# Kernel tuning notes

Measured on AMD Instinct MI355X. Metric: run time of the kernel, lower is better.

## Reference

```python
import jax, jax.numpy as jnp
import numpy as np

N, D, K = 32768, 128, 16
EPS = 1e-8  # torch cosine_similarity eps


def setup_inputs() -> dict:
    key = jax.random.key(0)
    k1, k2, kW1, kW2, kV = jax.random.split(key, 5)
    # xavier_normal std for [K, fan_in, fan_out]-style tensors (torch treats dim0 as batch? no:
    # xavier_normal_ on a 3D tensor uses fan_in = D*1? torch computes fan from dims 1.. with receptive field.
    # fan_in = size(1)*rf, fan_out = size(0)*rf where rf = prod(shape[2:]).
    def xavier_std(shape):
        rf = int(np.prod(shape[2:])) if len(shape) > 2 else 1
        fan_in = shape[1] * rf
        fan_out = shape[0] * rf
        return float(np.sqrt(2.0 / (fan_in + fan_out)))
    W1 = jax.random.normal(kW1, (K, D, D), jnp.float32) * xavier_std((K, D, D))
    W2 = jax.random.normal(kW2, (K, D, D), jnp.float32) * xavier_std((K, D, D))
    V = jax.random.normal(kV, (K, 2 * D, 1), jnp.float32) * xavier_std((K, 2 * D, 1))
    b = jnp.zeros((K,), jnp.float32)
    x_1 = jax.random.normal(k1, (N, D), jnp.float32)
    x_2 = jax.random.normal(k2, (N, D), jnp.float32)
    return {"x_1": x_1, "x_2": x_2, "W1": W1, "W2": W2, "V": V, "b": b}


def reference(x_1, x_2, W1, W2, V, b):
    # Batched version of the per-slice loop: one bmm per side instead of K matmuls.
    x1_t = jnp.einsum('nd,kde->kne', x_1, W1)  # [K, N, D]
    x2_t = jnp.einsum('nd,kde->kne', x_2, W2)  # [K, N, D]
    # torch.cosine_similarity(dim=-1): dot / (clamp(||a||, eps) * clamp(||b||, eps))
    num = jnp.sum(x1_t * x2_t, axis=-1)                      # [K, N]
    n1 = jnp.maximum(jnp.sqrt(jnp.sum(x1_t * x1_t, -1)), EPS)
    n2 = jnp.maximum(jnp.sqrt(jnp.sum(x2_t * x2_t, -1)), EPS)
    part1 = num / (n1 * n2)                                  # [K, N]
    x_cat = jnp.concatenate([x_1, x_2], axis=-1)             # [N, 2D]
    part2 = jnp.einsum('nc,kc->kn', x_cat, V[:, :, 0])       # [K, N]
    fea = part1 + part2 + b[:, None]                         # [K, N]
    return jax.nn.relu(fea.T)                                # [N, K]
```

## Files before the change

### kernel.cpp

```cpp
#include <hip/hip_runtime.h>


typedef __attribute__((ext_vector_type(8))) __bf16 bf16x8;
typedef __attribute__((ext_vector_type(8))) unsigned short us8;
typedef __attribute__((ext_vector_type(4))) float f32x4;

static __device__ __forceinline__ unsigned short f2bf(float f) {
  unsigned u = __float_as_uint(f);
  u += 0x7FFFu + ((u >> 16) & 1u);
  return (unsigned short)(u >> 16);
}

static __device__ __forceinline__ bf16x8 as_bf(us8 u) {
  bf16x8 r;
  __builtin_memcpy(&r, &u, sizeof(r));
  return r;
}

__global__ void ntn_prep(const float* __restrict__ W1, const float* __restrict__ W2,
                         const float* __restrict__ V,
                         unsigned short* __restrict__ wsW, unsigned short* __restrict__ wsV) {
  int t = blockIdx.x * 256 + threadIdx.x;
  if (t < 65536) {
    int u = t & 2047;
    int lane = u & 63, s = (u >> 6) & 3, et2 = (u >> 8) & 3, side = (u >> 10) & 1;
    int cc = t >> 11, h = cc & 1, k = cc >> 1;
    int q = lane >> 4, l15 = lane & 15;
    int et = h * 4 + et2;
    const float* W = side ? W2 : W1;
    const float* src = W + k * 16384 + (s * 32 + q * 8) * 128 + (et * 16 + l15);
    us8 r;
#pragma unroll
    for (int j = 0; j < 8; ++j) r[j] = f2bf(src[j * 128]);
    *(us8*)(wsW + (size_t)t * 8) = r;
  } else if (t < 66048) {
    int u = t - 65536;
    int lane = u & 63, cs = u >> 6;
    int q = lane >> 4, l15 = lane & 15;
    const float* src = V + l15 * 256 + cs * 32 + q * 8;
    us8 r;
#pragma unroll
    for (int j = 0; j < 8; ++j) r[j] = f2bf(src[j]);
    *(us8*)(wsV + (size_t)u * 8) = r;
  }
}

__global__ __launch_bounds__(256, 2) void ntn_main(
    const float* __restrict__ x1, const float* __restrict__ x2,
    const float* __restrict__ b,
    const unsigned short* __restrict__ wsW, const unsigned short* __restrict__ wsV,
    float* __restrict__ out) {
  __shared__ uint4 ldsW[2][2048];

  const int tid = threadIdx.x;
  const int lane = tid & 63, wave = tid >> 6;
  const int q = lane >> 4, l15 = lane & 15;
  const int kh = blockIdx.x & 1;
  const int rb = blockIdx.x >> 1;
  const int rowbase = rb * 128 + wave * 32;

  const f32x4 zero4 = {0.f, 0.f, 0.f, 0.f};

  auto stage = [&](int cc, int slot) {
    const unsigned short* src = wsW + (size_t)cc * 16384 + (size_t)(wave * 512 + lane) * 8;
    uint4* dst = &ldsW[slot][wave * 512];
#pragma unroll
    for (int i = 0; i < 8; ++i)
      __builtin_amdgcn_global_load_lds(
          (__attribute__((address_space(1))) void*)(void*)(src + i * 512),
          (__attribute__((address_space(3))) void*)(dst + i * 64), 16, 0, 0);
  };

  stage(kh * 16, 0);

  bf16x8 xb[2][2][4];
#pragma unroll
  for (int side = 0; side < 2; ++side) {
    const float* xp0 = side ? x2 : x1;
#pragma unroll
    for (int nt = 0; nt < 2; ++nt) {
#pragma unroll
      for (int s = 0; s < 4; ++s) {
        const float* p = xp0 + (size_t)(rowbase + nt * 16 + l15) * 128 + s * 32 + q * 8;
        float4 v0 = *(const float4*)p;
        float4 v1 = *(const float4*)(p + 4);
        us8 uu;
        uu[0] = f2bf(v0.x); uu[1] = f2bf(v0.y); uu[2] = f2bf(v0.z); uu[3] = f2bf(v0.w);
        uu[4] = f2bf(v1.x); uu[5] = f2bf(v1.y); uu[6] = f2bf(v1.z); uu[7] = f2bf(v1.w);
        xb[side][nt][s] = as_bf(uu);
      }
    }
  }

  f32x4 accP[2];
  {
    bf16x8 vf[8];
#pragma unroll
    for (int cs = 0; cs < 8; ++cs)
      vf[cs] = as_bf(*(const us8*)(wsV + (size_t)(cs * 64 + lane) * 8));
    float4 bv = *(const float4*)(b + q * 4);
#pragma unroll
    for (int nt = 0; nt < 2; ++nt) {
      f32x4 a = zero4;
#pragma unroll
      for (int cs = 0; cs < 8; ++cs)
        a = __builtin_amdgcn_mfma_f32_16x16x32_bf16(vf[cs], xb[cs >> 2][nt][cs & 3], a, 0, 0, 0);
      a.x += bv.x; a.y += bv.y; a.z += bv.z; a.w += bv.w;
      accP[nt] = a;
    }
  }

  float nm[2] = {0.f, 0.f}, q1[2] = {0.f, 0.f}, q2[2] = {0.f, 0.f};

  auto compute = [&](int slot) {
#pragma unroll
    for (int et = 0; et < 4; ++et) {
      bf16x8 wa[4], wb[4];
#pragma unroll
      for (int s = 0; s < 4; ++s) {
        wa[s] = as_bf(*(const us8*)&ldsW[slot][et * 256 + s * 64 + lane]);
        wb[s] = as_bf(*(const us8*)&ldsW[slot][1024 + et * 256 + s * 64 + lane]);
      }
#pragma unroll
      for (int nt = 0; nt < 2; ++nt) {
        f32x4 a1 = zero4, a2 = zero4;
#pragma unroll
        for (int s = 0; s < 4; ++s)
          a1 = __builtin_amdgcn_mfma_f32_16x16x32_bf16(wa[s], xb[0][nt][s], a1, 0, 0, 0);
#pragma unroll
        for (int s = 0; s < 4; ++s)
          a2 = __builtin_amdgcn_mfma_f32_16x16x32_bf16(wb[s], xb[1][nt][s], a2, 0, 0, 0);
        nm[nt] += a1.x * a2.x + a1.y * a2.y + a1.z * a2.z + a1.w * a2.w;
        q1[nt] += a1.x * a1.x + a1.y * a1.y + a1.z * a1.z + a1.w * a1.w;
        q2[nt] += a2.x * a2.x + a2.y * a2.y + a2.z * a2.z + a2.w * a2.w;
      }
    }
  };

#pragma unroll 1
  for (int kk = 0; kk < 8; ++kk) {
    const int cbase = kh * 16 + 2 * kk;
    __syncthreads();
    stage(cbase + 1, 1);
    compute(0);
    __syncthreads();
    if (kk < 7) stage(cbase + 2, 0);
    compute(1);

    const int k = kh * 8 + kk;
    const int qo = k >> 2;
    const int r  = k & 3;
#pragma unroll
    for (int nt = 0; nt < 2; ++nt) {
      float n = nm[nt], s1 = q1[nt], s2 = q2[nt];
      n  += __shfl_xor(n, 16);  n  += __shfl_xor(n, 32);
      s1 += __shfl_xor(s1, 16); s1 += __shfl_xor(s1, 32);
      s2 += __shfl_xor(s2, 16); s2 += __shfl_xor(s2, 32);
      float d1 = fmaxf(sqrtf(s1), 1e-8f);
      float d2 = fmaxf(sqrtf(s2), 1e-8f);
      float p1 = n / (d1 * d2);
      float pc = (r == 0) ? accP[nt].x : (r == 1) ? accP[nt].y
               : (r == 2) ? accP[nt].z : accP[nt].w;
      if (q == qo)
        out[(size_t)(rowbase + nt * 16 + l15) * 16 + k] = fmaxf(p1 + pc, 0.f);
      nm[nt] = 0.f; q1[nt] = 0.f; q2[nt] = 0.f;
    }
  }
}

extern "C" void kernel_launch(void* const* d_in, const int* in_sizes, int n_in,
                              void* d_out, int out_size, void* d_ws, size_t ws_size,
                              hipStream_t stream) {
  const float* x1 = (const float*)d_in[0];
  const float* x2 = (const float*)d_in[1];
  const float* W1 = (const float*)d_in[2];
  const float* W2 = (const float*)d_in[3];
  const float* V  = (const float*)d_in[4];
  const float* b  = (const float*)d_in[5];
  float* out = (float*)d_out;
  unsigned short* wsW = (unsigned short*)d_ws;
  unsigned short* wsV = wsW + (size_t)65536 * 8;

  ntn_prep<<<258, 256, 0, stream>>>(W1, W2, V, wsW, wsV);
  ntn_main<<<512, 256, 0, stream>>>(x1, x2, b, wsW, wsV, out);
}
```

Baseline: 119.5 us.

## Split weight staging into four half-chunk LDS buffers with vmcnt-based barriers

Splits each LDS weight stage into per-side halves and cycles them through four buffers. Explicit s_waitcnt vmcnt thresholds plus barriers let each global-to-LDS prefetch overlap two compute phases instead of one. MFMA sections are wrapped in s_setprio to favour matrix issue across waves. The cost is more barriers per step, extra registers to hold the side-A accumulators between phases, and correctness that depends on the hand-chosen vmcnt counts.

Measured after the change: 119.9 us. Within noise of the previous version (+0.4%).

```diff
diff --git a/kernel.cpp b/kernel.cpp
--- a/kernel.cpp
+++ b/kernel.cpp
@@ -15,6 +15,13 @@
   bf16x8 r;
   __builtin_memcpy(&r, &u, sizeof(r));
   return r;
+}
+
+template <int VM>
+static __device__ __forceinline__ void waitbar() {
+  asm volatile("s_waitcnt vmcnt(%0)" :: "i"(VM) : "memory");
+  __builtin_amdgcn_s_barrier();
+  __builtin_amdgcn_sched_barrier(0);
 }
 
 __global__ void ntn_prep(const float* __restrict__ W1, const float* __restrict__ W2,
@@ -50,7 +57,7 @@
     const float* __restrict__ b,
     const unsigned short* __restrict__ wsW, const unsigned short* __restrict__ wsV,
     float* __restrict__ out) {
-  __shared__ uint4 ldsW[2][2048];
+  __shared__ uint4 ldsH[4][1024];
 
   const int tid = threadIdx.x;
   const int lane = tid & 63, wave = tid >> 6;
@@ -61,17 +68,16 @@
 
   const f32x4 zero4 = {0.f, 0.f, 0.f, 0.f};
 
-  auto stage = [&](int cc, int slot) {
-    const unsigned short* src = wsW + (size_t)cc * 16384 + (size_t)(wave * 512 + lane) * 8;
-    uint4* dst = &ldsW[slot][wave * 512];
-#pragma unroll
-    for (int i = 0; i < 8; ++i)
+  auto stage = [&](int cc, int side, int slot) {
+    const unsigned short* src =
+        wsW + ((size_t)cc * 2048 + side * 1024 + wave * 256 + lane) * 8;
+    uint4* dst = &ldsH[slot][wave * 256];
+#pragma unroll
+    for (int i = 0; i < 4; ++i)
       __builtin_amdgcn_global_load_lds(
           (__attribute__((address_space(1))) void*)(void*)(src + i * 512),
           (__attribute__((address_space(3))) void*)(dst + i * 64), 16, 0, 0);
   };
-
-  stage(kh * 16, 0);
 
   bf16x8 xb[2][2][4];
 #pragma unroll
@@ -111,43 +117,52 @@
   }
 
   float nm[2] = {0.f, 0.f}, q1[2] = {0.f, 0.f}, q2[2] = {0.f, 0.f};
-
-  auto compute = [&](int slot) {
+  f32x4 a1[4][2];
+
+  auto computeA = [&](int slot) {
 #pragma unroll
     for (int et = 0; et < 4; ++et) {
-      bf16x8 wa[4], wb[4];
-#pragma unroll
-      for (int s = 0; s < 4; ++s) {
-        wa[s] = as_bf(*(const us8*)&ldsW[slot][et * 256 + s * 64 + lane]);
-        wb[s] = as_bf(*(const us8*)&ldsW[slot][1024 + et * 256 + s * 64 + lane]);
+      bf16x8 wa[4];
+#pragma unroll
+      for (int s = 0; s < 4; ++s)
+        wa[s] = as_bf(*(const us8*)&ldsH[slot][et * 256 + s * 64 + lane]);
+      __builtin_amdgcn_s_setprio(1);
+#pragma unroll
+      for (int nt = 0; nt < 2; ++nt) {
+        f32x4 a = zero4;
+#pragma unroll
+        for (int s = 0; s < 4; ++s)
+          a = __builtin_amdgcn_mfma_f32_16x16x32_bf16(wa[s], xb[0][nt][s], a, 0, 0, 0);
+        a1[et][nt] = a;
       }
+      __builtin_amdgcn_s_setprio(0);
+    }
+  };
+
+  auto computeB = [&](int slot) {
+#pragma unroll
+    for (int et = 0; et < 4; ++et) {
+      bf16x8 wb[4];
+#pragma unroll
+      for (int s = 0; s < 4; ++s)
+        wb[s] = as_bf(*(const us8*)&ldsH[slot][et * 256 + s * 64 + lane]);
+      __builtin_amdgcn_s_setprio(1);
 #pragma unroll
       for (int nt = 0; nt < 2; ++nt) {
-        f32x4 a1 = zero4, a2 = zero4;
-#pragma unroll
-        for (int s = 0; s < 4; ++s)
-          a1 = __builtin_amdgcn_mfma_f32_16x16x32_bf16(wa[s], xb[0][nt][s], a1, 0, 0, 0);
+        f32x4 a2 = zero4;
 #pragma unroll
         for (int s = 0; s < 4; ++s)
           a2 = __builtin_amdgcn_mfma_f32_16x16x32_bf16(wb[s], xb[1][nt][s], a2, 0, 0, 0);
-        nm[nt] += a1.x * a2.x + a1.y * a2.y + a1.z * a2.z + a1.w * a2.w;
-        q1[nt] += a1.x * a1.x + a1.y * a1.y + a1.z * a1.z + a1.w * a1.w;
+        f32x4 v1 = a1[et][nt];
+        nm[nt] += v1.x * a2.x + v1.y * a2.y + v1.z * a2.z + v1.w * a2.w;
+        q1[nt] += v1.x * v1.x + v1.y * v1.y + v1.z * v1.z + v1.w * v1.w;
         q2[nt] += a2.x * a2.x + a2.y * a2.y + a2.z * a2.z + a2.w * a2.w;
       }
-    }
-  };
-
-#pragma unroll 1
-  for (int kk = 0; kk < 8; ++kk) {
-    const int cbase = kh * 16 + 2 * kk;
-    __syncthreads();
-    stage(cbase + 1, 1);
-    compute(0);
-    __syncthreads();
-    if (kk < 7) stage(cbase + 2, 0);
-    compute(1);
-
-    const int k = kh * 8 + kk;
+      __builtin_amdgcn_s_setprio(0);
+    }
+  };
+
+  auto epilogue = [&](int k) {
     const int qo = k >> 2;
     const int r  = k & 3;
 #pragma unroll
@@ -165,7 +180,30 @@
         out[(size_t)(rowbase + nt * 16 + l15) * 16 + k] = fmaxf(p1 + pc, 0.f);
       nm[nt] = 0.f; q1[nt] = 0.f; q2[nt] = 0.f;
     }
-  }
+  };
+
+  {
+    const int c0 = kh * 16;
+    stage(c0, 0, 0);
+    stage(c0, 1, 1);
+  }
+
+#define KSTEP(V0, V1, V2, V3, DO23, C0, KIDX)                \
+  do {                                                       \
+    waitbar<V0>(); stage((C0) + 1, 0, 2); computeA(0);       \
+    waitbar<V1>(); stage((C0) + 1, 1, 3); computeB(1);       \
+    waitbar<V2>(); if (DO23) stage((C0) + 2, 0, 0); computeA(2); \
+    waitbar<V3>(); if (DO23) stage((C0) + 2, 1, 1); computeB(3); \
+    epilogue(KIDX);                                          \
+  } while (0)
+
+  { KSTEP(4, 4, 4, 4, true, kh * 16, kh * 8); }
+#pragma unroll 1
+  for (int kk = 1; kk < 7; ++kk) {
+    KSTEP(6, 6, 4, 4, true, kh * 16 + 2 * kk, kh * 8 + kk);
+  }
+  { KSTEP(6, 6, 4, 0, false, kh * 16 + 14, kh * 8 + 7); }
+#undef KSTEP
 }
 
 extern "C" void kernel_launch(void* const* d_in, const int* in_sizes, int n_in,
```
